# Kernel tuning notes

Hardware: AMD Instinct MI355X
Metric: run time of the kernel (lower is better)

The kernel has to match this reference:

```python
import jax, jax.numpy as jnp
import numpy as np

D_MODEL, D_HEAD, N_HEADS, N_KV_HEADS = 4096, 128, 32, 8
EPS = 1e-5
N = 2048


def rms_norm(x, w, eps):
    return x * jax.lax.rsqrt(jnp.mean(x * x, axis=-1, keepdims=True) + eps) * w


def rope_swap(x):
    # [x0, x1, x2, x3] -> [-x1, x0, -x3, x2]
    xp = x.reshape(x.shape[:-1] + (-1, 2))
    return jnp.stack([-xp[..., 1], xp[..., 0]], axis=-1).reshape(x.shape)


def rope_rotate(x, r_cos, r_sin):
    return x * r_cos + rope_swap(x) * r_sin


def setup_inputs() -> dict:
    key = jax.random.key(0)
    ks = jax.random.split(key, 8)
    sd = 1.0 / np.sqrt(D_MODEL)
    return {
        "x": jax.random.normal(ks[0], (N, D_MODEL), dtype=jnp.float32),
        "r_cos": jax.random.normal(ks[1], (N, D_HEAD), dtype=jnp.float32),
        "r_sin": jax.random.normal(ks[2], (N, D_HEAD), dtype=jnp.float32),
        "w_norm": jnp.ones((D_MODEL,), dtype=jnp.float32),
        "wq": jax.random.normal(ks[3], (D_MODEL, N_HEADS * D_HEAD), dtype=jnp.float32) * sd,
        "wk": jax.random.normal(ks[4], (D_MODEL, N_KV_HEADS * D_HEAD), dtype=jnp.float32) * sd,
        "wv": jax.random.normal(ks[5], (D_MODEL, N_KV_HEADS * D_HEAD), dtype=jnp.float32) * sd,
        "wo": jax.random.normal(ks[6], (D_MODEL, D_MODEL), dtype=jnp.float32) * sd,
    }


def reference(x, r_cos, r_sin, w_norm, wq, wk, wv, wo):
    n = x.shape[0]
    residual = x
    h = rms_norm(x, w_norm, EPS)

    # projections -> [n_heads, n, d_head]
    q = (h @ wq).reshape(n, N_HEADS, D_HEAD).transpose(1, 0, 2)
    k = (h @ wk).reshape(n, N_KV_HEADS, D_HEAD).transpose(1, 0, 2)
    v = (h @ wv).reshape(n, N_KV_HEADS, D_HEAD).transpose(1, 0, 2)

    # GQA: repeat kv heads
    reps = N_HEADS // N_KV_HEADS
    k = jnp.repeat(k, reps, axis=0)
    v = jnp.repeat(v, reps, axis=0)

    q = rope_rotate(q, r_cos, r_sin)
    k = rope_rotate(k, r_cos, r_sin)

    mask = jnp.where(
        jnp.tril(jnp.ones((n, n), dtype=bool)), 0.0, -jnp.inf
    ).astype(x.dtype)
    scores = jnp.einsum("hnd,hmd->hnm", q, k) / np.sqrt(D_HEAD).astype(np.float32) + mask
    a = jnp.einsum("hnm,hmd->hnd", jax.nn.softmax(scores, axis=-1), v)

    a = a.transpose(1, 0, 2).reshape(n, N_HEADS * D_HEAD)
    return residual + a @ wo
```

## Files before the change

kernel.cpp:

```cpp
#include <hip/hip_runtime.h>
#include <stdint.h>
#include <math.h>

#define TOK 2048
#define DMODEL 4096
#define QKV_LD 5120
#define KVB 64
#define PS_LD 72

typedef __attribute__((ext_vector_type(8))) short short8;
typedef __attribute__((ext_vector_type(4))) short short4v;
typedef __attribute__((ext_vector_type(8))) __bf16 bf16x8;
typedef __attribute__((ext_vector_type(4))) float f32x4;

__device__ __forceinline__ unsigned short f2bf(float f) {
  unsigned u = __float_as_uint(f);
  u += 0x7fffu + ((u >> 16) & 1u);
  return (unsigned short)(u >> 16);
}

__device__ __forceinline__ void gl16(const void* g, void* l) {
  __builtin_amdgcn_global_load_lds((__attribute__((address_space(1))) void*)g,
                                   (__attribute__((address_space(3))) void*)l,
                                   16, 0, 0);
}

__device__ __forceinline__ f32x4 mfma16(short8 a, short8 b, f32x4 c) {
  return __builtin_amdgcn_mfma_f32_16x16x32_bf16(__builtin_bit_cast(bf16x8, a),
                                                 __builtin_bit_cast(bf16x8, b),
                                                 c, 0, 0, 0);
}

__device__ __forceinline__ float fexp2(float x) {
  float r;
  asm("v_exp_f32 %0, %1" : "=v"(r) : "v"(x));
  return r;
}

template <int N>
__device__ __forceinline__ void waitvm() {
  if constexpr (N == 0) asm volatile("s_waitcnt vmcnt(0)" ::: "memory");
  else if constexpr (N == 3) asm volatile("s_waitcnt vmcnt(3)" ::: "memory");
  else if constexpr (N == 4) asm volatile("s_waitcnt vmcnt(4)" ::: "memory");
  else if constexpr (N == 8) asm volatile("s_waitcnt vmcnt(8)" ::: "memory");
  else static_assert(N == 0 || N == 3 || N == 4 || N == 8, "add literal");
}

__global__ __launch_bounds__(256) void k_rmsnorm(const float* __restrict__ x,
                                                 const float* __restrict__ w,
                                                 unsigned short* __restrict__ h) {
  const int row = blockIdx.x;
  const float* xr = x + (size_t)row * DMODEL;
  float4 v[4];
  float ss = 0.f;
#pragma unroll
  for (int i = 0; i < 4; ++i) {
    v[i] = *(const float4*)(xr + threadIdx.x * 4 + i * 1024);
    ss += v[i].x * v[i].x + v[i].y * v[i].y + v[i].z * v[i].z + v[i].w * v[i].w;
  }
#pragma unroll
  for (int m = 1; m < 64; m <<= 1) ss += __shfl_xor(ss, m, 64);
  __shared__ float ws4[4];
  if ((threadIdx.x & 63) == 0) ws4[threadIdx.x >> 6] = ss;
  __syncthreads();
  const float scale = rsqrtf((ws4[0] + ws4[1] + ws4[2] + ws4[3]) * (1.0f / DMODEL) + 1e-5f);
  unsigned short* hr = h + (size_t)row * DMODEL;
#pragma unroll
  for (int i = 0; i < 4; ++i) {
    int col = threadIdx.x * 4 + i * 1024;
    float4 wv = *(const float4*)(w + col);
    uint2 o;
    o.x = (unsigned)f2bf(v[i].x * scale * wv.x) | ((unsigned)f2bf(v[i].y * scale * wv.y) << 16);
    o.y = (unsigned)f2bf(v[i].z * scale * wv.z) | ((unsigned)f2bf(v[i].w * scale * wv.w) << 16);
    *(uint2*)(hr + col) = o;
  }
}

__global__ __launch_bounds__(256) void k_wconvert(const float* __restrict__ W,
                                                  unsigned short* __restrict__ WT,
                                                  int K, int N) {
  __shared__ unsigned short tile[64][65];
  const int n0 = blockIdx.x * 64, k0 = blockIdx.y * 64;
  const int t = threadIdx.x;
  {
    const int r = t >> 2, c0 = (t & 3) * 16;
    const float* src = W + (size_t)(k0 + r) * N + n0 + c0;
#pragma unroll
    for (int i = 0; i < 4; ++i) {
      float4 f = *(const float4*)(src + i * 4);
      tile[r][c0 + i * 4 + 0] = f2bf(f.x);
      tile[r][c0 + i * 4 + 1] = f2bf(f.y);
      tile[r][c0 + i * 4 + 2] = f2bf(f.z);
      tile[r][c0 + i * 4 + 3] = f2bf(f.w);
    }
  }
  __syncthreads();
  {
    const int n = t >> 2, c0 = (t & 3) * 16;
    unsigned short* dst = WT + (size_t)(n0 + n) * K + k0 + c0;
    unsigned short v[16];
#pragma unroll
    for (int i = 0; i < 16; ++i) v[i] = tile[c0 + i][n];
    uint4 o0, o1;
    o0.x = v[0] | ((unsigned)v[1] << 16);  o0.y = v[2] | ((unsigned)v[3] << 16);
    o0.z = v[4] | ((unsigned)v[5] << 16);  o0.w = v[6] | ((unsigned)v[7] << 16);
    o1.x = v[8] | ((unsigned)v[9] << 16);  o1.y = v[10] | ((unsigned)v[11] << 16);
    o1.z = v[12] | ((unsigned)v[13] << 16); o1.w = v[14] | ((unsigned)v[15] << 16);
    *(uint4*)dst = o0;
    *(uint4*)(dst + 8) = o1;
  }
}

__device__ __forceinline__ short8 rdfrag(const unsigned short* buf, int row, int kc) {
  return *(const short8*)((const char*)buf + row * 128 + ((kc ^ (row & 7)) << 4));
}

template <int BM, int BN, int HALF>
__device__ __forceinline__ void stage_half(const unsigned short* __restrict__ A,
                                           const unsigned short* __restrict__ BT,
                                           unsigned short* __restrict__ buf,
                                           int m0, int n0, int K, int kt, int tid) {
  constexpr int LA = BM / 64, LB = BN / 64;
  constexpr int H0A = LA / 2, H0B = (LB + 1) / 2;
  constexpr int A0 = HALF ? H0A : 0, A1 = HALF ? LA : H0A;
  constexpr int B0 = HALF ? H0B : 0, B1 = HALF ? LB : H0B;
  unsigned short* bbuf = buf + BM * 64;
#pragma unroll
  for (int i = A0; i < A1; ++i) {
    const int s = i * 512 + tid, row = s >> 3, ch = s & 7;
    gl16(A + (size_t)(m0 + row) * K + kt + ((ch ^ (row & 7)) << 3), (char*)buf + s * 16);
  }
#pragma unroll
  for (int i = B0; i < B1; ++i) {
    const int s = i * 512 + tid, row = s >> 3, ch = s & 7;
    gl16(BT + (size_t)(n0 + row) * K + kt + ((ch ^ (row & 7)) << 3), (char*)bbuf + s * 16);
  }
}

template <int BM, int BN, int MODE>
__global__ __launch_bounds__(512, 2) void k_gemm_big(const unsigned short* __restrict__ A,
                                                     const unsigned short* __restrict__ BT,
                                                     const float* __restrict__ resid,
                                                     void* __restrict__ Cout,
                                                     unsigned short* __restrict__ vtg,
                                                     const float* __restrict__ rc,
                                                     const float* __restrict__ rs,
                                                     int M, int N, int K) {
  extern __shared__ __align__(16) unsigned short lds[];
  constexpr int MREP = BM / 32;
  constexpr int NREP = BN / 64;
  constexpr int TILE = (BM + BN) * 64;
  constexpr int LA = BM / 64, LB = BN / 64;
  constexpr int H0 = LA / 2 + (LB + 1) / 2;

  const int tid = threadIdx.x, lane = tid & 63;
  const int w = tid >> 6, wm = w >> 2, wn = w & 3;
  const int lr = lane & 15, lh = lane >> 4;

  const int wg0 = blockIdx.x;
  const int xcd = wg0 & 7, l = wg0 >> 3;
  const int m0 = (((xcd >> 2) << 2) + (l >> 3)) * BM;
  const int n0 = (((xcd & 3) << 3) + (l & 7)) * BN;

  const f32x4 zf = {0.f, 0.f, 0.f, 0.f};
  f32x4 acc[MREP][NREP];
#pragma unroll
  for (int i = 0; i < MREP; ++i) {
#pragma unroll
    for (int j = 0; j < NREP; ++j) acc[i][j] = zf;
  }

  const int arow0 = wm * (BM / 2);
  const int brow0 = wn * (BN / 4);
  const int NT = K >> 6;
  int cur = 0;

  stage_half<BM, BN, 0>(A, BT, lds, m0, n0, K, 0, tid);
  stage_half<BM, BN, 1>(A, BT, lds, m0, n0, K, 0, tid);

  for (int t = 0; t < NT; ++t) {
    const unsigned short* abuf = lds + cur * TILE;
    const unsigned short* bbuf = abuf + BM * 64;
    unsigned short* nbuf = lds + (cur ^ 1) * TILE;
    const bool pre = (t + 1 < NT);
    const int ktn = (t + 1) << 6;

    short8 bfr[NREP], afr[4];
    if (pre) {
      stage_half<BM, BN, 0>(A, BT, nbuf, m0, n0, K, ktn, tid);
      waitvm<H0>();
    } else {
      waitvm<0>();
    }
    __builtin_amdgcn_s_barrier();
#pragma unroll
    for (int nr = 0; nr < NREP; ++nr) bfr[nr] = rdfrag(bbuf, brow0 + nr * 16 + lr, lh);
#pragma unroll
    for (int mi = 0; mi < 4; ++mi) afr[mi] = rdfrag(abuf, arow0 + mi * 16 + lr, lh);
    __builtin_amdgcn_s_setprio(1);
#pragma unroll
    for (int mi = 0; mi < 4; ++mi) {
#pragma unroll
      for (int nr = 0; nr < NREP; ++nr)
        acc[mi][nr] = mfma16(afr[mi], bfr[nr], acc[mi][nr]);
    }
    __builtin_amdgcn_s_setprio(0);
    if (pre) stage_half<BM, BN, 1>(A, BT, nbuf, m0, n0, K, ktn, tid);
#pragma unroll
    for (int mi = 0; mi < 4; ++mi) afr[mi] = rdfrag(abuf, arow0 + (4 + mi) * 16 + lr, lh);
    __builtin_amdgcn_s_setprio(1);
#pragma unroll
    for (int mi = 0; mi < 4; ++mi) {
#pragma unroll
      for (int nr = 0; nr < NREP; ++nr)
        acc[4 + mi][nr] = mfma16(afr[mi], bfr[nr], acc[4 + mi][nr]);
    }
    __builtin_amdgcn_s_setprio(0);
#pragma unroll
    for (int nr = 0; nr < NREP; ++nr) bfr[nr] = rdfrag(bbuf, brow0 + nr * 16 + lr, 4 + lh);
#pragma unroll
    for (int mi = 0; mi < 4; ++mi) afr[mi] = rdfrag(abuf, arow0 + mi * 16 + lr, 4 + lh);
    __builtin_amdgcn_s_setprio(1);
#pragma unroll
    for (int mi = 0; mi < 4; ++mi) {
#pragma unroll
      for (int nr = 0; nr < NREP; ++nr)
        acc[mi][nr] = mfma16(afr[mi], bfr[nr], acc[mi][nr]);
    }
    __builtin_amdgcn_s_setprio(0);
#pragma unroll
    for (int mi = 0; mi < 4; ++mi) afr[mi] = rdfrag(abuf, arow0 + (4 + mi) * 16 + lr, 4 + lh);
    asm volatile("s_waitcnt lgkmcnt(0)" ::: "memory");
    __builtin_amdgcn_s_barrier();
    __builtin_amdgcn_s_setprio(1);
#pragma unroll
    for (int mi = 0; mi < 4; ++mi) {
#pragma unroll
      for (int nr = 0; nr < NREP; ++nr)
        acc[4 + mi][nr] = mfma16(afr[mi], bfr[nr], acc[4 + mi][nr]);
    }
    __builtin_amdgcn_s_setprio(0);
    cur ^= 1;
  }

#pragma unroll
  for (int ai = 0; ai < MREP; ++ai) {
#pragma unroll
    for (int ni = 0; ni < NREP; ++ni) {
      const int colg = n0 + wn * (BN / 4) + ni * 16 + lr;
      const int rowg0 = m0 + wm * (BM / 2) + ai * 16 + 4 * lh;
      if (MODE == 1) {
#pragma unroll
        for (int r = 0; r < 4; ++r)
          ((float*)Cout)[(size_t)(rowg0 + r) * N + colg] =
              acc[ai][ni][r] + resid[(size_t)(rowg0 + r) * N + colg];
      } else if (colg >= 5120) {
        short4v o;
#pragma unroll
        for (int r = 0; r < 4; ++r) o[r] = (short)f2bf(acc[ai][ni][r]);
        *(short4v*)(vtg + (size_t)(colg - 5120) * TOK + rowg0) = o;
      } else {
        const int d = colg & 127;
#pragma unroll
        for (int r = 0; r < 4; ++r) {
          const int row = rowg0 + r;
          const float v = acc[ai][ni][r];
          const float p = __shfl_xor(v, 1, 64);
          const float c = rc[row * 128 + d];
          const float s = rs[row * 128 + d];
          const float y = (lr & 1) ? fmaf(p, s, v * c) : fmaf(-p, s, v * c);
          ((unsigned short*)Cout)[(size_t)row * QKV_LD + colg] = f2bf(y);
        }
      }
    }
  }
}

__global__ __launch_bounds__(256) void k_attn(const unsigned short* __restrict__ qkv,
                                              const unsigned short* __restrict__ vtg,
                                              unsigned short* __restrict__ aout) {
  extern __shared__ __align__(16) unsigned short sm[];
  unsigned short* const KsB = sm;
  unsigned short* const VtB = sm + 2 * KVB * 128;
  unsigned short* const Ps = sm + 4 * KVB * 128;
  const int head = blockIdx.y;
  const int hkv = head >> 2;
  const int tid = threadIdx.x, lane = tid & 63, w = tid >> 6;
  const int lr = lane & 15, lh = lane >> 4;
  const float scale2 = 0.08838834764831845f * 1.44269504088896340736f;
  const f32x4 zf = {0.f, 0.f, 0.f, 0.f};

  for (int half = 0; half < 2; ++half) {
    const int qt = half ? (31 - blockIdx.x) : blockIdx.x;
    const int q0 = qt * 64;

    short8 qf[4];
    {
      const unsigned short* qbase = qkv + (size_t)(q0 + w * 16 + lr) * QKV_LD + head * 128;
#pragma unroll
      for (int kd = 0; kd < 4; ++kd) qf[kd] = *(const short8*)(qbase + kd * 32 + lh * 8);
    }
    f32x4 oacc[8];
#pragma unroll
    for (int vt = 0; vt < 8; ++vt) oacc[vt] = zf;
    float Mr[4], Lp[4];
#pragma unroll
    for (int r = 0; r < 4; ++r) { Mr[r] = -INFINITY; Lp[r] = 0.f; }

    const int nt = qt + 1;
    int cur = 0;

    {
#pragma unroll
      for (int c = 0; c < 4; ++c) {
        const int s = c * 256 + w * 64 + lane;
        const int row = s >> 4, cp = s & 15;
        gl16(qkv + (size_t)row * QKV_LD + 4096 + hkv * 128 + ((cp ^ (row & 7)) * 8),
             (char*)KsB + (c * 256 + w * 64) * 16);
      }
#pragma unroll
      for (int c = 0; c < 4; ++c) {
        const int s = c * 256 + w * 64 + lane;
        const int row = s >> 3, cp = s & 7;
        gl16(vtg + (size_t)(hkv * 128 + row) * TOK + ((cp ^ (row & 7)) * 8),
             (char*)VtB + (c * 256 + w * 64) * 16);
      }
    }

    for (int t = 0; t < nt; ++t) {
      const unsigned short* Ks = KsB + cur * (KVB * 128);
      const unsigned short* Vt = VtB + cur * (128 * KVB);
      const int kv0 = t * KVB;
      if (t + 1 < nt) {
        unsigned short* Ksn = KsB + (cur ^ 1) * (KVB * 128);
        unsigned short* Vtn = VtB + (cur ^ 1) * (128 * KVB);
        const int kvn = (t + 1) * KVB;
#pragma unroll
        for (int c = 0; c < 4; ++c) {
          const int s = c * 256 + w * 64 + lane;
          const int row = s >> 4, cp = s & 15;
          gl16(qkv + (size_t)(kvn + row) * QKV_LD + 4096 + hkv * 128 + ((cp ^ (row & 7)) * 8),
               (char*)Ksn + (c * 256 + w * 64) * 16);
        }
#pragma unroll
        for (int c = 0; c < 4; ++c) {
          const int s = c * 256 + w * 64 + lane;
          const int row = s >> 3, cp = s & 7;
          gl16(vtg + (size_t)(hkv * 128 + row) * TOK + kvn + ((cp ^ (row & 7)) * 8),
               (char*)Vtn + (c * 256 + w * 64) * 16);
        }
        waitvm<8>();
      } else {
        waitvm<0>();
      }
      __builtin_amdgcn_s_barrier();

      f32x4 sacc[4];
#pragma unroll
      for (int ct = 0; ct < 4; ++ct) {
        sacc[ct] = zf;
        const int row = ct * 16 + lr;
#pragma unroll
        for (int kd = 0; kd < 4; ++kd) {
          const short8 kf = *(const short8*)((const char*)Ks + row * 256 +
                                             (((kd * 4 + lh) ^ (row & 7)) * 16));
          sacc[ct] = mfma16(qf[kd], kf, sacc[ct]);
        }
      }

      const bool diag = (t == qt);
      float sv[4][4], gmax[4];
#pragma unroll
      for (int r = 0; r < 4; ++r) {
        float s0 = sacc[0][r] * scale2;
        float s1 = sacc[1][r] * scale2;
        float s2 = sacc[2][r] * scale2;
        float s3 = sacc[3][r] * scale2;
        if (diag) {
          const int qrow = q0 + w * 16 + 4 * lh + r;
          if (kv0 + lr > qrow) s0 = -INFINITY;
          if (kv0 + 16 + lr > qrow) s1 = -INFINITY;
          if (kv0 + 32 + lr > qrow) s2 = -INFINITY;
          if (kv0 + 48 + lr > qrow) s3 = -INFINITY;
        }
        float tmax = fmaxf(fmaxf(s0, s1), fmaxf(s2, s3));
        tmax = fmaxf(tmax, __shfl_xor(tmax, 1, 16));
        tmax = fmaxf(tmax, __shfl_xor(tmax, 2, 16));
        tmax = fmaxf(tmax, __shfl_xor(tmax, 4, 16));
        tmax = fmaxf(tmax, __shfl_xor(tmax, 8, 16));
        gmax[r] = tmax;
        sv[r][0] = s0; sv[r][1] = s1; sv[r][2] = s2; sv[r][3] = s3;
      }
      const int cond = (gmax[0] <= Mr[0] + 8.f) && (gmax[1] <= Mr[1] + 8.f) &&
                       (gmax[2] <= Mr[2] + 8.f) && (gmax[3] <= Mr[3] + 8.f);
      if (!__all(cond)) {
        float scv[4];
#pragma unroll
        for (int r = 0; r < 4; ++r) {
          const float mnew = fmaxf(Mr[r], gmax[r]);
          scv[r] = fexp2(Mr[r] - mnew);
          Mr[r] = mnew;
          Lp[r] *= scv[r];
        }
#pragma unroll
        for (int vt = 0; vt < 8; ++vt) {
#pragma unroll
          for (int r = 0; r < 4; ++r) oacc[vt][r] *= scv[r];
        }
      }
      float pv[4][4];
#pragma unroll
      for (int r = 0; r < 4; ++r) {
        const float p0 = fexp2(sv[r][0] - Mr[r]);
        const float p1 = fexp2(sv[r][1] - Mr[r]);
        const float p2 = fexp2(sv[r][2] - Mr[r]);
        const float p3 = fexp2(sv[r][3] - Mr[r]);
        Lp[r] += (p0 + p1) + (p2 + p3);
        pv[r][0] = p0; pv[r][1] = p1; pv[r][2] = p2; pv[r][3] = p3;
      }

      unsigned short* pw = Ps + w * (16 * PS_LD);
#pragma unroll
      for (int r = 0; r < 4; ++r) {
#pragma unroll
        for (int ct = 0; ct < 4; ++ct)
          pw[(4 * lh + r) * PS_LD + ct * 16 + lr] = f2bf(pv[r][ct]);
      }
      asm volatile("s_waitcnt lgkmcnt(0)" ::: "memory");
      short8 pf[2];
      pf[0] = *(const short8*)(pw + lr * PS_LD + lh * 8);
      pf[1] = *(const short8*)(pw + lr * PS_LD + 32 + lh * 8);
      __builtin_amdgcn_s_setprio(1);
#pragma unroll
      for (int vt = 0; vt < 8; ++vt) {
        const int d = vt * 16 + lr;
#pragma unroll
        for (int kb = 0; kb < 2; ++kb) {
          const short8 vf = *(const short8*)((const char*)Vt + d * 128 +
                                             (((kb * 4 + lh) ^ (lr & 7)) * 16));
          oacc[vt] = mfma16(pf[kb], vf, oacc[vt]);
        }
      }
      __builtin_amdgcn_s_setprio(0);
      asm volatile("s_waitcnt lgkmcnt(0)" ::: "memory");
      __builtin_amdgcn_s_barrier();
      cur ^= 1;
    }

#pragma unroll
    for (int r = 0; r < 4; ++r) {
      float Ls = Lp[r];
      Ls += __shfl_xor(Ls, 1, 16);
      Ls += __shfl_xor(Ls, 2, 16);
      Ls += __shfl_xor(Ls, 4, 16);
      Ls += __shfl_xor(Ls, 8, 16);
      const float inv = 1.0f / Ls;
      const size_t rowoff = (size_t)(q0 + w * 16 + 4 * lh + r) * DMODEL + head * 128;
#pragma unroll
      for (int vt = 0; vt < 8; ++vt)
        aout[rowoff + vt * 16 + lr] = f2bf(oacc[vt][r] * inv);
    }
  }
}

extern "C" void kernel_launch(void* const* d_in, const int* in_sizes, int n_in,
                              void* d_out, int out_size, void* d_ws, size_t ws_size,
                              hipStream_t stream) {
  (void)in_sizes; (void)n_in; (void)out_size; (void)ws_size;
  const float* x     = (const float*)d_in[0];
  const float* r_cos = (const float*)d_in[1];
  const float* r_sin = (const float*)d_in[2];
  const float* wnorm = (const float*)d_in[3];
  const float* wq    = (const float*)d_in[4];
  const float* wk    = (const float*)d_in[5];
  const float* wv    = (const float*)d_in[6];
  const float* wo    = (const float*)d_in[7];

  unsigned short* bufA = (unsigned short*)d_ws;
  unsigned short* qkvb = bufA + (size_t)TOK * DMODEL;
  unsigned short* wT   = qkvb + (size_t)TOK * QKV_LD;
  unsigned short* vtg  = wT + (size_t)6144 * DMODEL;

  hipFuncSetAttribute((const void*)k_gemm_big<256, 192, 0>,
                      hipFuncAttributeMaxDynamicSharedMemorySize, 4 * (256 + 192) * 64);
  hipFuncSetAttribute((const void*)k_gemm_big<256, 128, 1>,
                      hipFuncAttributeMaxDynamicSharedMemorySize, 4 * (256 + 128) * 64);
  const int attn_lds = 4 * KVB * 128 * 2 + 4 * 16 * PS_LD * 2;
  hipFuncSetAttribute((const void*)k_attn,
                      hipFuncAttributeMaxDynamicSharedMemorySize, attn_lds);

  k_rmsnorm<<<TOK, 256, 0, stream>>>(x, wnorm, bufA);
  k_wconvert<<<dim3(64, 64), 256, 0, stream>>>(wq, wT, DMODEL, 4096);
  k_wconvert<<<dim3(16, 64), 256, 0, stream>>>(wk, wT + (size_t)4096 * DMODEL, DMODEL, 1024);
  k_wconvert<<<dim3(16, 64), 256, 0, stream>>>(wv, wT + (size_t)5120 * DMODEL, DMODEL, 1024);
  k_gemm_big<256, 192, 0><<<dim3(256), 512, 4 * (256 + 192) * 64, stream>>>(
      bufA, wT, nullptr, qkvb, vtg, r_cos, r_sin, TOK, 6144, DMODEL);
  k_wconvert<<<dim3(64, 64), 256, 0, stream>>>(wo, wT, DMODEL, 4096);
  k_attn<<<dim3(16, 32), 256, attn_lds, stream>>>(qkvb, vtg, bufA);
  k_gemm_big<256, 128, 1><<<dim3(256), 512, 4 * (256 + 128) * 64, stream>>>(
      bufA, wT, x, d_out, nullptr, nullptr, nullptr, TOK, DMODEL, DMODEL);
}
```

Before: 309.6 us.

## Simplify GEMM and attention pipelines to single-barrier prefetch, retile output GEMM

Both the GEMM and the attention loops now wait for the whole current tile, take one barrier, and only then issue the full prefetch of the next tile into the other buffer. This replaces the split half-tile staging with partial vmcnt waits and drops the trailing barrier at the end of each iteration. The output projection GEMM changes from 256x128 to 128x256 tiles, with a parametrised XCD-aware block mapping. The goal is fewer barriers and simpler scheduling, at the cost of less overlap between global loads and MFMA work inside each iteration.

After: 309.0 us. Within noise of the previous version (-0.2%).

```diff
diff --git a/kernel.cpp b/kernel.cpp
--- a/kernel.cpp
+++ b/kernel.cpp
@@ -37,13 +37,8 @@
   return r;
 }
 
-template <int N>
-__device__ __forceinline__ void waitvm() {
-  if constexpr (N == 0) asm volatile("s_waitcnt vmcnt(0)" ::: "memory");
-  else if constexpr (N == 3) asm volatile("s_waitcnt vmcnt(3)" ::: "memory");
-  else if constexpr (N == 4) asm volatile("s_waitcnt vmcnt(4)" ::: "memory");
-  else if constexpr (N == 8) asm volatile("s_waitcnt vmcnt(8)" ::: "memory");
-  else static_assert(N == 0 || N == 3 || N == 4 || N == 8, "add literal");
+__device__ __forceinline__ void waitvm0() {
+  asm volatile("s_waitcnt vmcnt(0)" ::: "memory");
 }
 
 __global__ __launch_bounds__(256) void k_rmsnorm(const float* __restrict__ x,
@@ -115,29 +110,26 @@
   return *(const short8*)((const char*)buf + row * 128 + ((kc ^ (row & 7)) << 4));
 }
 
-template <int BM, int BN, int HALF>
-__device__ __forceinline__ void stage_half(const unsigned short* __restrict__ A,
+template <int BM, int BN>
+__device__ __forceinline__ void stage_tile(const unsigned short* __restrict__ A,
                                            const unsigned short* __restrict__ BT,
                                            unsigned short* __restrict__ buf,
                                            int m0, int n0, int K, int kt, int tid) {
   constexpr int LA = BM / 64, LB = BN / 64;
-  constexpr int H0A = LA / 2, H0B = (LB + 1) / 2;
-  constexpr int A0 = HALF ? H0A : 0, A1 = HALF ? LA : H0A;
-  constexpr int B0 = HALF ? H0B : 0, B1 = HALF ? LB : H0B;
   unsigned short* bbuf = buf + BM * 64;
 #pragma unroll
-  for (int i = A0; i < A1; ++i) {
+  for (int i = 0; i < LA; ++i) {
     const int s = i * 512 + tid, row = s >> 3, ch = s & 7;
     gl16(A + (size_t)(m0 + row) * K + kt + ((ch ^ (row & 7)) << 3), (char*)buf + s * 16);
   }
 #pragma unroll
-  for (int i = B0; i < B1; ++i) {
+  for (int i = 0; i < LB; ++i) {
     const int s = i * 512 + tid, row = s >> 3, ch = s & 7;
     gl16(BT + (size_t)(n0 + row) * K + kt + ((ch ^ (row & 7)) << 3), (char*)bbuf + s * 16);
   }
 }
 
-template <int BM, int BN, int MODE>
+template <int BM, int BN, int MODE, int LOGN>
 __global__ __launch_bounds__(512, 2) void k_gemm_big(const unsigned short* __restrict__ A,
                                                      const unsigned short* __restrict__ BT,
                                                      const float* __restrict__ resid,
@@ -149,9 +141,8 @@
   extern __shared__ __align__(16) unsigned short lds[];
   constexpr int MREP = BM / 32;
   constexpr int NREP = BN / 64;
+  constexpr int MH = MREP / 2;
   constexpr int TILE = (BM + BN) * 64;
-  constexpr int LA = BM / 64, LB = BN / 64;
-  constexpr int H0 = LA / 2 + (LB + 1) / 2;
 
   const int tid = threadIdx.x, lane = tid & 63;
   const int w = tid >> 6, wm = w >> 2, wn = w & 3;
@@ -159,8 +150,9 @@
 
   const int wg0 = blockIdx.x;
   const int xcd = wg0 & 7, l = wg0 >> 3;
-  const int m0 = (((xcd >> 2) << 2) + (l >> 3)) * BM;
-  const int n0 = (((xcd & 3) << 3) + (l & 7)) * BN;
+  const int mch = (M / BM) >> 1;
+  const int m0 = ((xcd >> 2) * mch + (l >> LOGN)) * BM;
+  const int n0 = ((xcd & 3) * (1 << LOGN) + (l & ((1 << LOGN) - 1))) * BN;
 
   const f32x4 zf = {0.f, 0.f, 0.f, 0.f};
   f32x4 acc[MREP][NREP];
@@ -175,71 +167,39 @@
   const int NT = K >> 6;
   int cur = 0;
 
-  stage_half<BM, BN, 0>(A, BT, lds, m0, n0, K, 0, tid);
-  stage_half<BM, BN, 1>(A, BT, lds, m0, n0, K, 0, tid);
+  stage_tile<BM, BN>(A, BT, lds, m0, n0, K, 0, tid);
 
   for (int t = 0; t < NT; ++t) {
     const unsigned short* abuf = lds + cur * TILE;
     const unsigned short* bbuf = abuf + BM * 64;
-    unsigned short* nbuf = lds + (cur ^ 1) * TILE;
-    const bool pre = (t + 1 < NT);
-    const int ktn = (t + 1) << 6;
-
-    short8 bfr[NREP], afr[4];
-    if (pre) {
-      stage_half<BM, BN, 0>(A, BT, nbuf, m0, n0, K, ktn, tid);
-      waitvm<H0>();
-    } else {
-      waitvm<0>();
-    }
+    waitvm0();
     __builtin_amdgcn_s_barrier();
-#pragma unroll
-    for (int nr = 0; nr < NREP; ++nr) bfr[nr] = rdfrag(bbuf, brow0 + nr * 16 + lr, lh);
-#pragma unroll
-    for (int mi = 0; mi < 4; ++mi) afr[mi] = rdfrag(abuf, arow0 + mi * 16 + lr, lh);
-    __builtin_amdgcn_s_setprio(1);
-#pragma unroll
-    for (int mi = 0; mi < 4; ++mi) {
+    __builtin_amdgcn_sched_barrier(0);
+    if (t + 1 < NT)
+      stage_tile<BM, BN>(A, BT, lds + (cur ^ 1) * TILE, m0, n0, K, (t + 1) << 6, tid);
+
+#pragma unroll
+    for (int kk = 0; kk < 2; ++kk) {
+      short8 bfr[NREP];
 #pragma unroll
       for (int nr = 0; nr < NREP; ++nr)
-        acc[mi][nr] = mfma16(afr[mi], bfr[nr], acc[mi][nr]);
-    }
-    __builtin_amdgcn_s_setprio(0);
-    if (pre) stage_half<BM, BN, 1>(A, BT, nbuf, m0, n0, K, ktn, tid);
-#pragma unroll
-    for (int mi = 0; mi < 4; ++mi) afr[mi] = rdfrag(abuf, arow0 + (4 + mi) * 16 + lr, lh);
-    __builtin_amdgcn_s_setprio(1);
-#pragma unroll
-    for (int mi = 0; mi < 4; ++mi) {
-#pragma unroll
-      for (int nr = 0; nr < NREP; ++nr)
-        acc[4 + mi][nr] = mfma16(afr[mi], bfr[nr], acc[4 + mi][nr]);
-    }
-    __builtin_amdgcn_s_setprio(0);
-#pragma unroll
-    for (int nr = 0; nr < NREP; ++nr) bfr[nr] = rdfrag(bbuf, brow0 + nr * 16 + lr, 4 + lh);
-#pragma unroll
-    for (int mi = 0; mi < 4; ++mi) afr[mi] = rdfrag(abuf, arow0 + mi * 16 + lr, 4 + lh);
-    __builtin_amdgcn_s_setprio(1);
-#pragma unroll
-    for (int mi = 0; mi < 4; ++mi) {
-#pragma unroll
-      for (int nr = 0; nr < NREP; ++nr)
-        acc[mi][nr] = mfma16(afr[mi], bfr[nr], acc[mi][nr]);
-    }
-    __builtin_amdgcn_s_setprio(0);
-#pragma unroll
-    for (int mi = 0; mi < 4; ++mi) afr[mi] = rdfrag(abuf, arow0 + (4 + mi) * 16 + lr, 4 + lh);
-    asm volatile("s_waitcnt lgkmcnt(0)" ::: "memory");
-    __builtin_amdgcn_s_barrier();
-    __builtin_amdgcn_s_setprio(1);
-#pragma unroll
-    for (int mi = 0; mi < 4; ++mi) {
-#pragma unroll
-      for (int nr = 0; nr < NREP; ++nr)
-        acc[4 + mi][nr] = mfma16(afr[mi], bfr[nr], acc[4 + mi][nr]);
-    }
-    __builtin_amdgcn_s_setprio(0);
+        bfr[nr] = rdfrag(bbuf, brow0 + nr * 16 + lr, kk * 4 + lh);
+#pragma unroll
+      for (int mh = 0; mh < 2; ++mh) {
+        short8 afr[MH];
+#pragma unroll
+        for (int mi = 0; mi < MH; ++mi)
+          afr[mi] = rdfrag(abuf, arow0 + (mh * MH + mi) * 16 + lr, kk * 4 + lh);
+        __builtin_amdgcn_s_setprio(1);
+#pragma unroll
+        for (int mi = 0; mi < MH; ++mi) {
+#pragma unroll
+          for (int nr = 0; nr < NREP; ++nr)
+            acc[mh * MH + mi][nr] = mfma16(afr[mi], bfr[nr], acc[mh * MH + mi][nr]);
+        }
+        __builtin_amdgcn_s_setprio(0);
+      }
+    }
     cur ^= 1;
   }
 
@@ -290,6 +250,26 @@
   const float scale2 = 0.08838834764831845f * 1.44269504088896340736f;
   const f32x4 zf = {0.f, 0.f, 0.f, 0.f};
 
+  auto stageKV = [&](int kvt, int buf) {
+    unsigned short* Ksn = KsB + buf * (KVB * 128);
+    unsigned short* Vtn = VtB + buf * (128 * KVB);
+    const int kvn = kvt * KVB;
+#pragma unroll
+    for (int c = 0; c < 4; ++c) {
+      const int s = c * 256 + w * 64 + lane;
+      const int row = s >> 4, cp = s & 15;
+      gl16(qkv + (size_t)(kvn + row) * QKV_LD + 4096 + hkv * 128 + ((cp ^ (row & 7)) * 8),
+           (char*)Ksn + (c * 256 + w * 64) * 16);
+    }
+#pragma unroll
+    for (int c = 0; c < 4; ++c) {
+      const int s = c * 256 + w * 64 + lane;
+      const int row = s >> 3, cp = s & 7;
+      gl16(vtg + (size_t)(hkv * 128 + row) * TOK + kvn + ((cp ^ (row & 7)) * 8),
+           (char*)Vtn + (c * 256 + w * 64) * 16);
+    }
+  };
+
   for (int half = 0; half < 2; ++half) {
     const int qt = half ? (31 - blockIdx.x) : blockIdx.x;
     const int q0 = qt * 64;
@@ -309,51 +289,16 @@
 
     const int nt = qt + 1;
     int cur = 0;
-
-    {
-#pragma unroll
-      for (int c = 0; c < 4; ++c) {
-        const int s = c * 256 + w * 64 + lane;
-        const int row = s >> 4, cp = s & 15;
-        gl16(qkv + (size_t)row * QKV_LD + 4096 + hkv * 128 + ((cp ^ (row & 7)) * 8),
-             (char*)KsB + (c * 256 + w * 64) * 16);
-      }
-#pragma unroll
-      for (int c = 0; c < 4; ++c) {
-        const int s = c * 256 + w * 64 + lane;
-        const int row = s >> 3, cp = s & 7;
-        gl16(vtg + (size_t)(hkv * 128 + row) * TOK + ((cp ^ (row & 7)) * 8),
-             (char*)VtB + (c * 256 + w * 64) * 16);
-      }
-    }
+    stageKV(0, 0);
 
     for (int t = 0; t < nt; ++t) {
       const unsigned short* Ks = KsB + cur * (KVB * 128);
       const unsigned short* Vt = VtB + cur * (128 * KVB);
       const int kv0 = t * KVB;
-      if (t + 1 < nt) {
-        unsigned short* Ksn = KsB + (cur ^ 1) * (KVB * 128);
-        unsigned short* Vtn = VtB + (cur ^ 1) * (128 * KVB);
-        const int kvn = (t + 1) * KVB;
-#pragma unroll
-        for (int c = 0; c < 4; ++c) {
-          const int s = c * 256 + w * 64 + lane;
-          const int row = s >> 4, cp = s & 15;
-          gl16(qkv + (size_t)(kvn + row) * QKV_LD + 4096 + hkv * 128 + ((cp ^ (row & 7)) * 8),
-               (char*)Ksn + (c * 256 + w * 64) * 16);
-        }
-#pragma unroll
-        for (int c = 0; c < 4; ++c) {
-          const int s = c * 256 + w * 64 + lane;
-          const int row = s >> 3, cp = s & 7;
-          gl16(vtg + (size_t)(hkv * 128 + row) * TOK + kvn + ((cp ^ (row & 7)) * 8),
-               (char*)Vtn + (c * 256 + w * 64) * 16);
-        }
-        waitvm<8>();
-      } else {
-        waitvm<0>();
-      }
+      waitvm0();
       __builtin_amdgcn_s_barrier();
+      __builtin_amdgcn_sched_barrier(0);
+      if (t + 1 < nt) stageKV(t + 1, cur ^ 1);
 
       f32x4 sacc[4];
 #pragma unroll
@@ -442,8 +387,6 @@
         }
       }
       __builtin_amdgcn_s_setprio(0);
-      asm volatile("s_waitcnt lgkmcnt(0)" ::: "memory");
-      __builtin_amdgcn_s_barrier();
       cur ^= 1;
     }
 
@@ -460,6 +403,8 @@
       for (int vt = 0; vt < 8; ++vt)
         aout[rowoff + vt * 16 + lr] = f2bf(oacc[vt][r] * inv);
     }
+    __builtin_amdgcn_s_barrier();
+    __builtin_amdgcn_sched_barrier(0);
   }
 }
 
@@ -481,10 +426,10 @@
   unsigned short* wT   = qkvb + (size_t)TOK * QKV_LD;
   unsigned short* vtg  = wT + (size_t)6144 * DMODEL;
 
-  hipFuncSetAttribute((const void*)k_gemm_big<256, 192, 0>,
+  hipFuncSetAttribute((const void*)k_gemm_big<256, 192, 0, 3>,
                       hipFuncAttributeMaxDynamicSharedMemorySize, 4 * (256 + 192) * 64);
-  hipFuncSetAttribute((const void*)k_gemm_big<256, 128, 1>,
-                      hipFuncAttributeMaxDynamicSharedMemorySize, 4 * (256 + 128) * 64);
+  hipFuncSetAttribute((const void*)k_gemm_big<128, 256, 1, 2>,
+                      hipFuncAttributeMaxDynamicSharedMemorySize, 4 * (128 + 256) * 64);
   const int attn_lds = 4 * KVB * 128 * 2 + 4 * 16 * PS_LD * 2;
   hipFuncSetAttribute((const void*)k_attn,
                       hipFuncAttributeMaxDynamicSharedMemorySize, attn_lds);
@@ -493,10 +438,10 @@
   k_wconvert<<<dim3(64, 64), 256, 0, stream>>>(wq, wT, DMODEL, 4096);
   k_wconvert<<<dim3(16, 64), 256, 0, stream>>>(wk, wT + (size_t)4096 * DMODEL, DMODEL, 1024);
   k_wconvert<<<dim3(16, 64), 256, 0, stream>>>(wv, wT + (size_t)5120 * DMODEL, DMODEL, 1024);
-  k_gemm_big<256, 192, 0><<<dim3(256), 512, 4 * (256 + 192) * 64, stream>>>(
+  k_gemm_big<256, 192, 0, 3><<<dim3(256), 512, 4 * (256 + 192) * 64, stream>>>(
       bufA, wT, nullptr, qkvb, vtg, r_cos, r_sin, TOK, 6144, DMODEL);
   k_wconvert<<<dim3(64, 64), 256, 0, stream>>>(wo, wT, DMODEL, 4096);
   k_attn<<<dim3(16, 32), 256, attn_lds, stream>>>(qkvb, vtg, bufA);
-  k_gemm_big<256, 128, 1><<<dim3(256), 512, 4 * (256 + 128) * 64, stream>>>(
+  k_gemm_big<128, 256, 1, 2><<<dim3(256), 512, 4 * (128 + 256) * 64, stream>>>(
       bufA, wT, x, d_out, nullptr, nullptr, nullptr, TOK, DMODEL, DMODEL);
 }
```
